# Performance work log

Measured on AMD Instinct MI355X. Metric: run time of the kernel, lower is better.

The kernel has to match this reference:

```python
import jax, jax.numpy as jnp
import numpy as np

N = 5
RANK = 3
IMW = IMH = 1024
S = IMW * IMH
RANKLIST = [1] + [RANK] * (N - 1) + [1]  # [1,3,3,3,3,1]


def _xavier_std(shape):
    # torch xavier_normal_ on a 3D tensor (a, b, c): fan_in = b*c, fan_out = a*c
    a, b, c = shape
    fan_in, fan_out = b * c, a * c
    return float(np.sqrt(2.0 / (fan_in + fan_out)))


def setup_inputs() -> dict:
    key = jax.random.key(0)
    keys = jax.random.split(key, N + 1)
    inp = {"z": jax.random.normal(keys[0], (S,), dtype=jnp.float32)}
    for n in range(N):
        shp = (RANKLIST[n], S, RANKLIST[n + 1])
        inp[f"TT{n}"] = jax.random.normal(keys[n + 1], shp, dtype=jnp.float32) * _xavier_std(shp)
    return inp


def reference(z, TT0, TT1, TT2, TT3, TT4):
    # V[k] = z @ TT[k] : contract the s axis -> (r_k, r_{k+1}); tiny matrices.
    f = jnp.einsum('s,rsq->rq', z, TT0)          # (1, 3)
    for core in (TT1, TT2, TT3):
        f = f @ jnp.einsum('s,rsq->rq', z, core)  # (1, 3)
    # Last factor: the slice TT[N-1][:, :, 0] itself (NOT contracted with z).
    f = f @ TT4[:, :, 0]                          # (1, s)
    return f.reshape(-1)                          # (s,)
```

## Files before the change

kernel.cpp:

```cpp
#include <hip/hip_runtime.h>

#define SDIM (1024 * 1024)
#define GROUPS (SDIM / 4)
#define GPT 4
#define CHUNKS (GROUPS / (256 * GPT))
#define NPLANE 10

__global__ __launch_bounds__(256) void ftt_k1(
    const float* __restrict__ z,
    const float* __restrict__ t0,
    const float* __restrict__ t1,
    const float* __restrict__ t2,
    const float* __restrict__ t3,
    float* __restrict__ partials)
{
    const int plane = blockIdx.y;

    const float* base;
    if (plane == 0) {
        base = t0;
    } else {
        const int pk = plane - 1;
        const int k = pk / 3;
        const float* tk = (k == 0) ? t1 : (k == 1) ? t2 : t3;
        base = tk + (pk % 3) * (3 * SDIM);
    }

    const int g0 = blockIdx.x * (256 * GPT) + threadIdx.x;
    float a0 = 0.0f, a1 = 0.0f, a2 = 0.0f;

    #pragma unroll
    for (int it = 0; it < GPT; ++it) {
        const int g = g0 + it * 256;
        const float4 z4 = reinterpret_cast<const float4*>(z)[g];
        const float4* p = reinterpret_cast<const float4*>(base + 12 * g);
        const float4 c0 = p[0], c1 = p[1], c2 = p[2];
        a0 += z4.x * c0.x + z4.y * c0.w + z4.z * c1.z + z4.w * c2.y;
        a1 += z4.x * c0.y + z4.y * c1.x + z4.z * c1.w + z4.w * c2.z;
        a2 += z4.x * c0.z + z4.y * c1.y + z4.z * c2.x + z4.w * c2.w;
    }

    #pragma unroll
    for (int off = 32; off > 0; off >>= 1) {
        a0 += __shfl_down(a0, off, 64);
        a1 += __shfl_down(a1, off, 64);
        a2 += __shfl_down(a2, off, 64);
    }

    __shared__ float red[4][3];
    const int lane = threadIdx.x & 63;
    const int wave = threadIdx.x >> 6;
    if (lane == 0) { red[wave][0] = a0; red[wave][1] = a1; red[wave][2] = a2; }
    __syncthreads();
    if (threadIdx.x < 3) {
        const int c = threadIdx.x;
        const float s = red[0][c] + red[1][c] + red[2][c] + red[3][c];
        partials[(plane * CHUNKS + blockIdx.x) * 4 + c] = s;
    }
}

__global__ __launch_bounds__(256) void ftt_k2(
    const float* __restrict__ partials,
    float* __restrict__ fvec)
{
    __shared__ float red[NPLANE * 3][8];
    const int job = threadIdx.x >> 3;
    const int sub = threadIdx.x & 7;
    if (job < NPLANE * 3) {
        const int plane = job / 3, c = job % 3;
        float s = 0.0f;
        const int b0 = sub * (CHUNKS / 8);
        #pragma unroll 4
        for (int b = b0; b < b0 + (CHUNKS / 8); ++b)
            s += partials[(plane * CHUNKS + b) * 4 + c];
        red[job][sub] = s;
    }
    __syncthreads();

    if (threadIdx.x == 0) {
        float sum[NPLANE * 3];
        #pragma unroll
        for (int i = 0; i < NPLANE * 3; ++i) {
            float t = 0.0f;
            #pragma unroll
            for (int g = 0; g < 8; ++g) t += red[i][g];
            sum[i] = t;
        }
        float f0 = sum[0], f1 = sum[1], f2 = sum[2];
        #pragma unroll
        for (int k = 0; k < 3; ++k) {
            const float* V = &sum[3 + k * 9];
            const float n0 = f0 * V[0] + f1 * V[3] + f2 * V[6];
            const float n1 = f0 * V[1] + f1 * V[4] + f2 * V[7];
            const float n2 = f0 * V[2] + f1 * V[5] + f2 * V[8];
            f0 = n0; f1 = n1; f2 = n2;
        }
        fvec[0] = f0; fvec[1] = f1; fvec[2] = f2;
    }
}

__global__ __launch_bounds__(256) void ftt_k3(
    const float* __restrict__ t4,
    const float* __restrict__ fvec,
    float* __restrict__ out)
{
    const int i = blockIdx.x * blockDim.x + threadIdx.x;
    const float f0 = fvec[0], f1 = fvec[1], f2 = fvec[2];
    const float4 a = reinterpret_cast<const float4*>(t4)[i];
    const float4 b = reinterpret_cast<const float4*>(t4 + SDIM)[i];
    const float4 c = reinterpret_cast<const float4*>(t4 + 2 * SDIM)[i];
    float4 o;
    o.x = f0 * a.x + f1 * b.x + f2 * c.x;
    o.y = f0 * a.y + f1 * b.y + f2 * c.y;
    o.z = f0 * a.z + f1 * b.z + f2 * c.z;
    o.w = f0 * a.w + f1 * b.w + f2 * c.w;
    reinterpret_cast<float4*>(out)[i] = o;
}

extern "C" void kernel_launch(void* const* d_in, const int* in_sizes, int n_in,
                              void* d_out, int out_size, void* d_ws, size_t ws_size,
                              hipStream_t stream)
{
    const float* z  = (const float*)d_in[0];
    const float* t0 = (const float*)d_in[1];
    const float* t1 = (const float*)d_in[2];
    const float* t2 = (const float*)d_in[3];
    const float* t3 = (const float*)d_in[4];
    const float* t4 = (const float*)d_in[5];
    float* out = (float*)d_out;

    float* partials = (float*)d_ws;
    float* fvec     = partials + NPLANE * CHUNKS * 4;

    ftt_k1<<<dim3(CHUNKS, NPLANE), 256, 0, stream>>>(z, t0, t1, t2, t3, partials);
    ftt_k2<<<1, 256, 0, stream>>>(partials, fvec);
    ftt_k3<<<SDIM / 4 / 256, 256, 0, stream>>>(t4, fvec, out);
}
```

Measured before the change: 167.9 us.

## Fuse all ten planes per block with shared z tile and coalesced streaming

The first kernel now processes all ten rank planes in a single block over a 2048-element span of s. z is staged once in LDS and reused across planes, and each plane's data is read as fully coalesced float4 streams, with the per-thread residue-3 pattern handled by rotating accumulators. This removes the separate per-plane grid and the redundant z reads. It also reduces the block count to 512 with 512 threads each. Partials are stored in the output buffer in a transposed layout so the reduction kernel can use vector loads, which raises register pressure from 30 accumulators and more shuffle reduction work per block.

```diff
diff --git a/kernel.cpp b/kernel.cpp
--- a/kernel.cpp
+++ b/kernel.cpp
@@ -1,12 +1,13 @@
 #include <hip/hip_runtime.h>
 
 #define SDIM (1024 * 1024)
-#define GROUPS (SDIM / 4)
-#define GPT 4
-#define CHUNKS (GROUPS / (256 * GPT))
 #define NPLANE 10
+#define K1_THREADS 512
+#define NBLK 512
+#define SPAN_S 2048
+#define STREAM_F4 512
 
-__global__ __launch_bounds__(256) void ftt_k1(
+__global__ __launch_bounds__(K1_THREADS, 4) void ftt_k1(
     const float* __restrict__ z,
     const float* __restrict__ t0,
     const float* __restrict__ t1,
@@ -14,48 +15,92 @@
     const float* __restrict__ t3,
     float* __restrict__ partials)
 {
-    const int plane = blockIdx.y;
+    const int t = threadIdx.x;
+    const int blk = blockIdx.x;
 
-    const float* base;
-    if (plane == 0) {
-        base = t0;
-    } else {
-        const int pk = plane - 1;
-        const int k = pk / 3;
-        const float* tk = (k == 0) ? t1 : (k == 1) ? t2 : t3;
-        base = tk + (pk % 3) * (3 * SDIM);
+    __shared__ __align__(16) float zl[SPAN_S];
+    reinterpret_cast<float4*>(zl)[t] =
+        reinterpret_cast<const float4*>(z)[blk * (SPAN_S / 4) + t];
+    __syncthreads();
+
+    float z0[3], z1[3], zB[3], zC[3];
+    #pragma unroll
+    for (int m = 0; m < 3; ++m) {
+        const int e0 = 2048 * m + 4 * t;
+        const int s0 = e0 / 3;
+        const int r  = e0 % 3;
+        z0[m] = zl[s0];
+        z1[m] = zl[s0 + 1];
+        zB[m] = (r <= 1) ? z0[m] : z1[m];
+        zC[m] = (r == 0) ? z0[m] : z1[m];
     }
 
-    const int g0 = blockIdx.x * (256 * GPT) + threadIdx.x;
-    float a0 = 0.0f, a1 = 0.0f, a2 = 0.0f;
+    float B[NPLANE][3];
+    #pragma unroll
+    for (int p = 0; p < NPLANE; ++p) { B[p][0] = 0.f; B[p][1] = 0.f; B[p][2] = 0.f; }
+
+    const float* bases[NPLANE];
+    bases[0] = t0;
+    bases[1] = t1;  bases[2] = t1 + 3 * SDIM;  bases[3] = t1 + 6 * SDIM;
+    bases[4] = t2;  bases[5] = t2 + 3 * SDIM;  bases[6] = t2 + 6 * SDIM;
+    bases[7] = t3;  bases[8] = t3 + 3 * SDIM;  bases[9] = t3 + 6 * SDIM;
+    const int off = blk * (SPAN_S * 3);
 
     #pragma unroll
-    for (int it = 0; it < GPT; ++it) {
-        const int g = g0 + it * 256;
-        const float4 z4 = reinterpret_cast<const float4*>(z)[g];
-        const float4* p = reinterpret_cast<const float4*>(base + 12 * g);
-        const float4 c0 = p[0], c1 = p[1], c2 = p[2];
-        a0 += z4.x * c0.x + z4.y * c0.w + z4.z * c1.z + z4.w * c2.y;
-        a1 += z4.x * c0.y + z4.y * c1.x + z4.z * c1.w + z4.w * c2.z;
-        a2 += z4.x * c0.z + z4.y * c1.y + z4.z * c2.x + z4.w * c2.w;
+    for (int p = 0; p < NPLANE; ++p) {
+        const float4* pf = reinterpret_cast<const float4*>(bases[p] + off);
+        const float4 v0 = pf[t];
+        const float4 v1 = pf[t + STREAM_F4];
+        const float4 v2 = pf[t + 2 * STREAM_F4];
+        B[p][0] += v0.x * z0[0] + v0.w * z1[0];
+        B[p][1] += v0.y * zB[0];
+        B[p][2] += v0.z * zC[0];
+
+        B[p][2] += v1.x * z0[1] + v1.w * z1[1];
+        B[p][0] += v1.y * zB[1];
+        B[p][1] += v1.z * zC[1];
+
+        B[p][1] += v2.x * z0[2] + v2.w * z1[2];
+        B[p][2] += v2.y * zB[2];
+        B[p][0] += v2.z * zC[2];
+    }
+
+    const int rT = t % 3;
+    float a[NPLANE][3];
+    #pragma unroll
+    for (int p = 0; p < NPLANE; ++p) {
+        a[p][0] = (rT == 0) ? B[p][0] : (rT == 1) ? B[p][2] : B[p][1];
+        a[p][1] = (rT == 0) ? B[p][1] : (rT == 1) ? B[p][0] : B[p][2];
+        a[p][2] = (rT == 0) ? B[p][2] : (rT == 1) ? B[p][1] : B[p][0];
     }
 
     #pragma unroll
-    for (int off = 32; off > 0; off >>= 1) {
-        a0 += __shfl_down(a0, off, 64);
-        a1 += __shfl_down(a1, off, 64);
-        a2 += __shfl_down(a2, off, 64);
+    for (int sh = 32; sh > 0; sh >>= 1) {
+        #pragma unroll
+        for (int p = 0; p < NPLANE; ++p) {
+            a[p][0] += __shfl_down(a[p][0], sh, 64);
+            a[p][1] += __shfl_down(a[p][1], sh, 64);
+            a[p][2] += __shfl_down(a[p][2], sh, 64);
+        }
     }
 
-    __shared__ float red[4][3];
-    const int lane = threadIdx.x & 63;
-    const int wave = threadIdx.x >> 6;
-    if (lane == 0) { red[wave][0] = a0; red[wave][1] = a1; red[wave][2] = a2; }
+    __shared__ float red[K1_THREADS / 64][NPLANE * 3];
+    const int lane = t & 63, wave = t >> 6;
+    if (lane == 0) {
+        #pragma unroll
+        for (int p = 0; p < NPLANE; ++p) {
+            red[wave][p * 3 + 0] = a[p][0];
+            red[wave][p * 3 + 1] = a[p][1];
+            red[wave][p * 3 + 2] = a[p][2];
+        }
+    }
     __syncthreads();
-    if (threadIdx.x < 3) {
-        const int c = threadIdx.x;
-        const float s = red[0][c] + red[1][c] + red[2][c] + red[3][c];
-        partials[(plane * CHUNKS + blockIdx.x) * 4 + c] = s;
+    if (t < NPLANE * 3) {
+        const int p = t / 3, q = t % 3;
+        float s = 0.f;
+        #pragma unroll
+        for (int w = 0; w < K1_THREADS / 64; ++w) s += red[w][t];
+        partials[(q * NPLANE + p) * NBLK + blk] = s;
     }
 }
 
@@ -63,17 +108,19 @@
     const float* __restrict__ partials,
     float* __restrict__ fvec)
 {
-    __shared__ float red[NPLANE * 3][8];
-    const int job = threadIdx.x >> 3;
+    __shared__ float red[32][9];
+    const int row = threadIdx.x >> 3;
     const int sub = threadIdx.x & 7;
-    if (job < NPLANE * 3) {
-        const int plane = job / 3, c = job % 3;
-        float s = 0.0f;
-        const int b0 = sub * (CHUNKS / 8);
-        #pragma unroll 4
-        for (int b = b0; b < b0 + (CHUNKS / 8); ++b)
-            s += partials[(plane * CHUNKS + b) * 4 + c];
-        red[job][sub] = s;
+    if (row < NPLANE * 3) {
+        const float4* pr = reinterpret_cast<const float4*>(partials + row * NBLK)
+                           + sub * (NBLK / 4 / 8);
+        float s0 = 0.f, s1 = 0.f, s2 = 0.f, s3 = 0.f;
+        #pragma unroll
+        for (int i = 0; i < NBLK / 4 / 8; ++i) {
+            const float4 v = pr[i];
+            s0 += v.x; s1 += v.y; s2 += v.z; s3 += v.w;
+        }
+        red[row][sub] = (s0 + s1) + (s2 + s3);
     }
     __syncthreads();
 
@@ -81,18 +128,18 @@
         float sum[NPLANE * 3];
         #pragma unroll
         for (int i = 0; i < NPLANE * 3; ++i) {
-            float t = 0.0f;
+            float v = 0.f;
             #pragma unroll
-            for (int g = 0; g < 8; ++g) t += red[i][g];
-            sum[i] = t;
+            for (int g = 0; g < 8; ++g) v += red[i][g];
+            sum[i] = v;
         }
-        float f0 = sum[0], f1 = sum[1], f2 = sum[2];
+        float f0 = sum[0], f1 = sum[NPLANE], f2 = sum[2 * NPLANE];
         #pragma unroll
         for (int k = 0; k < 3; ++k) {
-            const float* V = &sum[3 + k * 9];
-            const float n0 = f0 * V[0] + f1 * V[3] + f2 * V[6];
-            const float n1 = f0 * V[1] + f1 * V[4] + f2 * V[7];
-            const float n2 = f0 * V[2] + f1 * V[5] + f2 * V[8];
+            const int pb = 1 + k * 3;
+            const float n0 = f0 * sum[0 * NPLANE + pb + 0] + f1 * sum[0 * NPLANE + pb + 1] + f2 * sum[0 * NPLANE + pb + 2];
+            const float n1 = f0 * sum[1 * NPLANE + pb + 0] + f1 * sum[1 * NPLANE + pb + 1] + f2 * sum[1 * NPLANE + pb + 2];
+            const float n2 = f0 * sum[2 * NPLANE + pb + 0] + f1 * sum[2 * NPLANE + pb + 1] + f2 * sum[2 * NPLANE + pb + 2];
             f0 = n0; f1 = n1; f2 = n2;
         }
         fvec[0] = f0; fvec[1] = f1; fvec[2] = f2;
@@ -129,10 +176,10 @@
     const float* t4 = (const float*)d_in[5];
     float* out = (float*)d_out;
 
-    float* partials = (float*)d_ws;
-    float* fvec     = partials + NPLANE * CHUNKS * 4;
+    float* partials = (float*)d_out;
+    float* fvec     = (float*)d_ws;
 
-    ftt_k1<<<dim3(CHUNKS, NPLANE), 256, 0, stream>>>(z, t0, t1, t2, t3, partials);
+    ftt_k1<<<NBLK, K1_THREADS, 0, stream>>>(z, t0, t1, t2, t3, partials);
     ftt_k2<<<1, 256, 0, stream>>>(partials, fvec);
     ftt_k3<<<SDIM / 4 / 256, 256, 0, stream>>>(t4, fvec, out);
 }
```

After: 186.9 us. +11.3%, slower.

## Coalesce TT plane loads and stage z in shared memory

Applied to the files above, without the earlier changes.

Changes the reduction kernel's access pattern. Adjacent threads now read adjacent float4s of each TT plane, where before each thread read 48 contiguous bytes at a 48-byte stride. The matching z values are staged in LDS and picked per thread by residue-mod-3 index logic, and the three accumulators are rotated back into channel order before the wave reduction. This aims at better coalescing of the dominant memory stream. In exchange it adds an LDS load, a barrier, and some select logic.

```diff
diff --git a/kernel.cpp b/kernel.cpp
--- a/kernel.cpp
+++ b/kernel.cpp
@@ -5,6 +5,7 @@
 #define GPT 4
 #define CHUNKS (GROUPS / (256 * GPT))
 #define NPLANE 10
+#define CHUNK_F4 (256 * GPT * 3)
 
 __global__ __launch_bounds__(256) void ftt_k1(
     const float* __restrict__ z,
@@ -15,6 +16,8 @@
     float* __restrict__ partials)
 {
     const int plane = blockIdx.y;
+    const int bx = blockIdx.x;
+    const int t = threadIdx.x;
 
     const float* base;
     if (plane == 0) {
@@ -26,19 +29,61 @@
         base = tk + (pk % 3) * (3 * SDIM);
     }
 
-    const int g0 = blockIdx.x * (256 * GPT) + threadIdx.x;
-    float a0 = 0.0f, a1 = 0.0f, a2 = 0.0f;
+    __shared__ __align__(16) float zl[256 * GPT * 4];
+    {
+        const float4* zf4 = reinterpret_cast<const float4*>(z) + bx * (256 * GPT);
+        float4* zs = reinterpret_cast<float4*>(zl);
+        #pragma unroll
+        for (int k = 0; k < GPT; ++k) zs[t + 256 * k] = zf4[t + 256 * k];
+    }
+    __syncthreads();
+
+    int dq[3]; bool sB[3], sC[3];
+    #pragma unroll
+    for (int m = 0; m < 3; ++m) {
+        const int e0 = 1024 * m + 4 * t;
+        dq[m] = e0 / 3;
+        const int r0 = e0 % 3;
+        sB[m] = (r0 <= 1);
+        sC[m] = (r0 == 0);
+    }
+
+    const float4* pf = reinterpret_cast<const float4*>(base) + bx * CHUNK_F4;
+
+    float B0 = 0.f, B1 = 0.f, B2 = 0.f;
 
     #pragma unroll
     for (int it = 0; it < GPT; ++it) {
-        const int g = g0 + it * 256;
-        const float4 z4 = reinterpret_cast<const float4*>(z)[g];
-        const float4* p = reinterpret_cast<const float4*>(base + 12 * g);
-        const float4 c0 = p[0], c1 = p[1], c2 = p[2];
-        a0 += z4.x * c0.x + z4.y * c0.w + z4.z * c1.z + z4.w * c2.y;
-        a1 += z4.x * c0.y + z4.y * c1.x + z4.z * c1.w + z4.w * c2.z;
-        a2 += z4.x * c0.z + z4.y * c1.y + z4.z * c2.x + z4.w * c2.w;
+        const int fb = it * 768;
+        const float4 v0 = pf[fb + t];
+        const float4 v1 = pf[fb + 256 + t];
+        const float4 v2 = pf[fb + 512 + t];
+        const int zo = 1024 * it;
+
+        {
+            const float z0 = zl[dq[0] + zo], z1 = zl[dq[0] + zo + 1];
+            B0 += v0.x * z0 + v0.w * z1;
+            B1 += v0.y * (sB[0] ? z0 : z1);
+            B2 += v0.z * (sC[0] ? z0 : z1);
+        }
+        {
+            const float z0 = zl[dq[1] + zo], z1 = zl[dq[1] + zo + 1];
+            B1 += v1.x * z0 + v1.w * z1;
+            B2 += v1.y * (sB[1] ? z0 : z1);
+            B0 += v1.z * (sC[1] ? z0 : z1);
+        }
+        {
+            const float z0 = zl[dq[2] + zo], z1 = zl[dq[2] + zo + 1];
+            B2 += v2.x * z0 + v2.w * z1;
+            B0 += v2.y * (sB[2] ? z0 : z1);
+            B1 += v2.z * (sC[2] ? z0 : z1);
+        }
     }
+
+    const int ri = t % 3;
+    float a0 = (ri == 0) ? B0 : (ri == 1) ? B2 : B1;
+    float a1 = (ri == 0) ? B1 : (ri == 1) ? B0 : B2;
+    float a2 = (ri == 0) ? B2 : (ri == 1) ? B1 : B0;
 
     #pragma unroll
     for (int off = 32; off > 0; off >>= 1) {
@@ -48,14 +93,13 @@
     }
 
     __shared__ float red[4][3];
-    const int lane = threadIdx.x & 63;
-    const int wave = threadIdx.x >> 6;
+    const int lane = t & 63;
+    const int wave = t >> 6;
     if (lane == 0) { red[wave][0] = a0; red[wave][1] = a1; red[wave][2] = a2; }
     __syncthreads();
-    if (threadIdx.x < 3) {
-        const int c = threadIdx.x;
-        const float s = red[0][c] + red[1][c] + red[2][c] + red[3][c];
-        partials[(plane * CHUNKS + blockIdx.x) * 4 + c] = s;
+    if (t < 3) {
+        const float s = red[0][t] + red[1][t] + red[2][t] + red[3][t];
+        partials[(plane * CHUNKS + bx) * 4 + t] = s;
     }
 }
 
```

After: 169.6 us. No clear change (+1.0%).

## Process all ten planes per thread to reuse z loads, partials in output buffer

Applied to the files above, without the earlier changes.

Each thread now loads its z float4 once and contracts it against all ten core planes, instead of each plane's blocks reloading z. The grid becomes one dimension of 1024 blocks with one group per thread. Partials are written into the output buffer, which the last kernel overwrites, so the workspace only holds fvec. The trade-off is high register pressure from 30 accumulators and 30 wave-level shuffle reductions per wave, and there are fewer blocks in flight to hide memory latency.

```diff
diff --git a/kernel.cpp b/kernel.cpp
--- a/kernel.cpp
+++ b/kernel.cpp
@@ -2,8 +2,7 @@
 
 #define SDIM (1024 * 1024)
 #define GROUPS (SDIM / 4)
-#define GPT 4
-#define CHUNKS (GROUPS / (256 * GPT))
+#define NBLK 1024
 #define NPLANE 10
 
 __global__ __launch_bounds__(256) void ftt_k1(
@@ -14,48 +13,52 @@
     const float* __restrict__ t3,
     float* __restrict__ partials)
 {
-    const int plane = blockIdx.y;
+    const int g = blockIdx.x * 256 + threadIdx.x;
+    const float4 z4 = reinterpret_cast<const float4*>(z)[g];
 
-    const float* base;
-    if (plane == 0) {
-        base = t0;
-    } else {
-        const int pk = plane - 1;
-        const int k = pk / 3;
-        const float* tk = (k == 0) ? t1 : (k == 1) ? t2 : t3;
-        base = tk + (pk % 3) * (3 * SDIM);
-    }
+    const float* bases[NPLANE];
+    bases[0] = t0;
+    bases[1] = t1;  bases[2] = t1 + 3 * SDIM;  bases[3] = t1 + 6 * SDIM;
+    bases[4] = t2;  bases[5] = t2 + 3 * SDIM;  bases[6] = t2 + 6 * SDIM;
+    bases[7] = t3;  bases[8] = t3 + 3 * SDIM;  bases[9] = t3 + 6 * SDIM;
 
-    const int g0 = blockIdx.x * (256 * GPT) + threadIdx.x;
-    float a0 = 0.0f, a1 = 0.0f, a2 = 0.0f;
-
+    float a0[NPLANE], a1[NPLANE], a2[NPLANE];
     #pragma unroll
-    for (int it = 0; it < GPT; ++it) {
-        const int g = g0 + it * 256;
-        const float4 z4 = reinterpret_cast<const float4*>(z)[g];
-        const float4* p = reinterpret_cast<const float4*>(base + 12 * g);
-        const float4 c0 = p[0], c1 = p[1], c2 = p[2];
-        a0 += z4.x * c0.x + z4.y * c0.w + z4.z * c1.z + z4.w * c2.y;
-        a1 += z4.x * c0.y + z4.y * c1.x + z4.z * c1.w + z4.w * c2.z;
-        a2 += z4.x * c0.z + z4.y * c1.y + z4.z * c2.x + z4.w * c2.w;
+    for (int p = 0; p < NPLANE; ++p) {
+        const float4* pf = reinterpret_cast<const float4*>(bases[p]) + 3 * g;
+        const float4 c0 = pf[0], c1 = pf[1], c2 = pf[2];
+        a0[p] = z4.x * c0.x + z4.y * c0.w + z4.z * c1.z + z4.w * c2.y;
+        a1[p] = z4.x * c0.y + z4.y * c1.x + z4.z * c1.w + z4.w * c2.z;
+        a2[p] = z4.x * c0.z + z4.y * c1.y + z4.z * c2.x + z4.w * c2.w;
     }
 
     #pragma unroll
     for (int off = 32; off > 0; off >>= 1) {
-        a0 += __shfl_down(a0, off, 64);
-        a1 += __shfl_down(a1, off, 64);
-        a2 += __shfl_down(a2, off, 64);
+        #pragma unroll
+        for (int p = 0; p < NPLANE; ++p) {
+            a0[p] += __shfl_down(a0[p], off, 64);
+            a1[p] += __shfl_down(a1[p], off, 64);
+            a2[p] += __shfl_down(a2[p], off, 64);
+        }
     }
 
-    __shared__ float red[4][3];
+    __shared__ float red[4][NPLANE * 3];
     const int lane = threadIdx.x & 63;
     const int wave = threadIdx.x >> 6;
-    if (lane == 0) { red[wave][0] = a0; red[wave][1] = a1; red[wave][2] = a2; }
+    if (lane == 0) {
+        #pragma unroll
+        for (int p = 0; p < NPLANE; ++p) {
+            red[wave][p * 3 + 0] = a0[p];
+            red[wave][p * 3 + 1] = a1[p];
+            red[wave][p * 3 + 2] = a2[p];
+        }
+    }
     __syncthreads();
-    if (threadIdx.x < 3) {
-        const int c = threadIdx.x;
-        const float s = red[0][c] + red[1][c] + red[2][c] + red[3][c];
-        partials[(plane * CHUNKS + blockIdx.x) * 4 + c] = s;
+    if (threadIdx.x < NPLANE * 3) {
+        const int p = threadIdx.x / 3, q = threadIdx.x % 3;
+        const float s = red[0][threadIdx.x] + red[1][threadIdx.x]
+                      + red[2][threadIdx.x] + red[3][threadIdx.x];
+        partials[(p * NBLK + blockIdx.x) * 4 + q] = s;
     }
 }
 
@@ -69,10 +72,10 @@
     if (job < NPLANE * 3) {
         const int plane = job / 3, c = job % 3;
         float s = 0.0f;
-        const int b0 = sub * (CHUNKS / 8);
+        const int b0 = sub * (NBLK / 8);
         #pragma unroll 4
-        for (int b = b0; b < b0 + (CHUNKS / 8); ++b)
-            s += partials[(plane * CHUNKS + b) * 4 + c];
+        for (int b = b0; b < b0 + (NBLK / 8); ++b)
+            s += partials[(plane * NBLK + b) * 4 + c];
         red[job][sub] = s;
     }
     __syncthreads();
@@ -129,10 +132,10 @@
     const float* t4 = (const float*)d_in[5];
     float* out = (float*)d_out;
 
-    float* partials = (float*)d_ws;
-    float* fvec     = partials + NPLANE * CHUNKS * 4;
+    float* partials = (float*)d_out;
+    float* fvec     = (float*)d_ws;
 
-    ftt_k1<<<dim3(CHUNKS, NPLANE), 256, 0, stream>>>(z, t0, t1, t2, t3, partials);
+    ftt_k1<<<NBLK, 256, 0, stream>>>(z, t0, t1, t2, t3, partials);
     ftt_k2<<<1, 256, 0, stream>>>(partials, fvec);
     ftt_k3<<<SDIM / 4 / 256, 256, 0, stream>>>(t4, fvec, out);
 }
```

After: 176.0 us. 4.8% more time.
